# Performance work log

Hardware: AMD Instinct MI355X
Metric: run time of the kernel (lower is better)

Reference implementation:

```python
import jax, jax.numpy as jnp
import numpy as np

BUCKET_SIZE = 64  # init kwarg bucket_size
DIM = 64          # init kwarg dim (per-head dim, used for scaling)


def setup_inputs() -> dict:
    key = jax.random.key(0)
    kq, kk = jax.random.split(key)
    q = jax.random.normal(kq, (32, 8192, 64), dtype=jnp.float32)
    k = jax.random.normal(kk, (32, 8192, 64), dtype=jnp.float32)
    return {"q": q, "k": k}


def _cumavg(t):
    # cumulative average along the sequence axis (axis=1)
    r = jnp.arange(1, t.shape[1] + 1, dtype=t.dtype)
    return jnp.cumsum(t, axis=1) / r[None, :, None]


def reference(q, k):
    bh, n, d = q.shape
    buckets = n // BUCKET_SIZE
    kv_buckets = k.shape[1] // BUCKET_SIZE

    # bucket the cumulative averages: [bh, buckets, bucket_size, d]
    q_r = _cumavg(q).reshape(bh, buckets, BUCKET_SIZE, d)
    k_r = _cumavg(k).reshape(bh, kv_buckets, BUCKET_SIZE, d)

    sq = q_r[:, :, 0]                                   # [bh, buckets, d]
    sk = k_r.sum(axis=2)                                # [bh, kv_buckets, d]
    sk = jnp.pad(sk, ((0, 0), (1, 0), (0, 0)))          # pad one zero bucket row at front

    R = jnp.einsum('bie,bje->bij', sq, sk) * (DIM ** -0.5)  # [bh, buckets, kv_buckets+1]

    rows = jnp.arange(buckets)[:, None]
    cols = jnp.arange(kv_buckets + 1)[None, :]
    neg = -jnp.finfo(R.dtype).max
    # masked_fill: for row i, columns i+1..buckets set to -max (cols > rows)
    R = jnp.where(cols > rows, neg, R)
    R = jax.nn.softmax(R, axis=-1)
    # tril(diagonal=-1): keep entries with col < row
    R = jnp.where(cols < rows, R, jnp.zeros((), R.dtype))
    return R
```

## Files before the change

kernel.cpp:

```cpp
#include <hip/hip_runtime.h>
#include <cstddef>

constexpr int BH = 32;
constexpr int N  = 8192;
constexpr int D  = 64;
constexpr int BK = 64;
constexpr int NB = 128;
constexpr int NC = 129;

typedef float v4f __attribute__((ext_vector_type(4)));

__global__ __launch_bounds__(256) void kA(const float* __restrict__ q,
                                          const float* __restrict__ k,
                                          float* __restrict__ qsum,
                                          float* __restrict__ ksum,
                                          float* __restrict__ kw,
                                          float* __restrict__ qfirst,
                                          float* __restrict__ W) {
  const int j = blockIdx.x, b = blockIdx.y;
  const int tid  = threadIdx.x;
  const int f    = tid & 15;
  const int rr   = tid >> 4;
  const int w    = tid >> 6;
  const int lane = tid & 63;
  const int base = j * BK;
  const size_t ob = ((size_t)b * NB + j) * D;

  const v4f* q4 = (const v4f*)(q + ((size_t)b * N + base) * D);
  const v4f* k4 = (const v4f*)(k + ((size_t)b * N + base) * D);

  v4f vq[4], vk[4];
#pragma unroll
  for (int p = 0; p < 4; ++p) vq[p] = __builtin_nontemporal_load(&q4[(16 * p + rr) * 16 + f]);
#pragma unroll
  for (int p = 0; p < 4; ++p) vk[p] = __builtin_nontemporal_load(&k4[(16 * p + rr) * 16 + f]);

  float x = 1.0f / (float)(base + lane + 1);
#pragma unroll
  for (int s = 1; s < 64; s <<= 1) {
    const float y = __shfl_down(x, s, 64);
    if (lane + s < 64) x += y;
  }
  float tw[4];
#pragma unroll
  for (int p = 0; p < 4; ++p) tw[p] = __shfl(x, 16 * p + rr, 64);

  float aq[4] = {0, 0, 0, 0}, ak[4] = {0, 0, 0, 0}, aw[4] = {0, 0, 0, 0};
#pragma unroll
  for (int p = 0; p < 4; ++p) {
    aq[0] += vq[p].x; aq[1] += vq[p].y; aq[2] += vq[p].z; aq[3] += vq[p].w;
    ak[0] += vk[p].x; ak[1] += vk[p].y; ak[2] += vk[p].z; ak[3] += vk[p].w;
    aw[0] += vk[p].x * tw[p]; aw[1] += vk[p].y * tw[p];
    aw[2] += vk[p].z * tw[p]; aw[3] += vk[p].w * tw[p];
  }

#pragma unroll
  for (int c = 0; c < 4; ++c) {
    aq[c] += __shfl_xor(aq[c], 16, 64); aq[c] += __shfl_xor(aq[c], 32, 64);
    ak[c] += __shfl_xor(ak[c], 16, 64); ak[c] += __shfl_xor(ak[c], 32, 64);
    aw[c] += __shfl_xor(aw[c], 16, 64); aw[c] += __shfl_xor(aw[c], 32, 64);
  }

  __shared__ float red[3][4][D];
  if (lane < 16) {
    ((float4*)&red[0][w][0])[f] = make_float4(aq[0], aq[1], aq[2], aq[3]);
    ((float4*)&red[1][w][0])[f] = make_float4(ak[0], ak[1], ak[2], ak[3]);
    ((float4*)&red[2][w][0])[f] = make_float4(aw[0], aw[1], aw[2], aw[3]);
  }
  if (rr == 0) {
    ((float4*)(qfirst + ob))[f] = make_float4(vq[0].x, vq[0].y, vq[0].z, vq[0].w);
  }
  if (tid == 0 && b == 0) W[j] = x;
  __syncthreads();

  if (tid < 192) {
    const int arr = tid >> 6, d = tid & 63;
    const float s = red[arr][0][d] + red[arr][1][d] + red[arr][2][d] + red[arr][3][d];
    float* dst = (arr == 0) ? qsum : (arr == 1) ? ksum : kw;
    dst[ob + d] = s;
  }
}

__global__ __launch_bounds__(256) void kB(const float* __restrict__ qsum,
                                          const float* __restrict__ ksum,
                                          const float* __restrict__ kw,
                                          const float* __restrict__ qfirst,
                                          const float* __restrict__ W,
                                          float* __restrict__ sq,
                                          float* __restrict__ skp) {
  const int side = blockIdx.x;
  const int b    = blockIdx.y;
  const int tid  = threadIdx.x;
  const int d    = tid & 63;
  const int jg   = tid >> 6;

  __shared__ float buf[NB * D];
  __shared__ float tot[4 * D];
  __shared__ float Wl[NB];

  const float* src = (side == 0 ? qsum : ksum) + (size_t)b * NB * D;
  {
    const float4* g4 = (const float4*)src;
    float4* l4 = (float4*)buf;
    for (int u = tid; u < NB * D / 4; u += 256) l4[u] = g4[u];
    if (side == 1 && tid < NB) Wl[tid] = W[tid];
  }
  __syncthreads();

  float t0 = 0.0f;
  for (int jj = 0; jj < 32; ++jj) t0 += buf[(jg * 32 + jj) * D + d];
  tot[jg * D + d] = t0;
  __syncthreads();

  float pre = 0.0f;
  for (int g = 0; g < jg; ++g) pre += tot[g * D + d];

  if (side == 0) {
    for (int jj = 0; jj < 32; ++jj) {
      const int j = jg * 32 + jj;
      const size_t o = ((size_t)b * NB + j) * D + d;
      sq[o] = (pre + qfirst[o]) / (float)(j * BK + 1);
      pre += buf[j * D + d];
    }
  } else {
    if (tid < D) skp[(size_t)b * NC * D + tid] = 0.0f;
    for (int jj = 0; jj < 32; ++jj) {
      const int j = jg * 32 + jj;
      const size_t o = ((size_t)b * NB + j) * D + d;
      skp[((size_t)b * NC + j + 1) * D + d] = pre * Wl[j] + kw[o];
      pre += buf[j * D + d];
    }
  }
}

__global__ __launch_bounds__(256) void kC(const float* __restrict__ sq,
                                          const float* __restrict__ skp,
                                          float* __restrict__ out) {
  const int tile = blockIdx.x, b = blockIdx.y;
  const int tid = threadIdx.x;
  const int jp = tid & 63, rep = tid >> 6;
  const int T0 = tile * 8;
  const int rows = T0 + 8;

  __shared__ float skpS[NB * D];
  __shared__ float sqs[8 * D];

  {
    const float4* g4 = (const float4*)(skp + (size_t)b * NC * D);
    for (int u = tid; u < rows * 16; u += 256) {
      const int row = u >> 4, f = u & 15;
      ((float4*)skpS)[row * 16 + ((f + row) & 15)] = g4[u];
    }
    if (tid < 128)
      ((float4*)sqs)[tid] = ((const float4*)(sq + ((size_t)b * NB + T0) * D))[tid];
  }
  __syncthreads();

  float acc0[2] = {0, 0}, acc1[2] = {0, 0};
  const float4* sk4 = (const float4*)skpS;
  const float4* sq4 = (const float4*)sqs;
#pragma unroll
  for (int d4 = 0; d4 < 16; ++d4) {
    const int slot = (d4 + jp) & 15;
    const float4 k0 = sk4[jp * 16 + slot];
    const float4 k1 = sk4[(jp + 64) * 16 + slot];
#pragma unroll
    for (int ii = 0; ii < 2; ++ii) {
      const float4 s = sq4[(rep * 2 + ii) * 16 + d4];
      acc0[ii] += s.x * k0.x + s.y * k0.y + s.z * k0.z + s.w * k0.w;
      acc1[ii] += s.x * k1.x + s.y * k1.y + s.z * k1.z + s.w * k1.w;
    }
  }

#pragma unroll
  for (int ii = 0; ii < 2; ++ii) {
    const int i = T0 + rep * 2 + ii;
    const int j0 = jp, j1 = jp + 64;
    const float v0 = acc0[ii] * 0.125f, v1 = acc1[ii] * 0.125f;
    const bool val0 = (j0 <= i), val1 = (j1 <= i);
    float m = fmaxf(val0 ? v0 : -3.402823466e38f, val1 ? v1 : -3.402823466e38f);
#pragma unroll
    for (int s = 1; s < 64; s <<= 1) m = fmaxf(m, __shfl_xor(m, s, 64));
    const float e0 = val0 ? __expf(v0 - m) : 0.0f;
    const float e1 = val1 ? __expf(v1 - m) : 0.0f;
    float ss = e0 + e1;
#pragma unroll
    for (int s = 1; s < 64; s <<= 1) ss += __shfl_xor(ss, s, 64);
    const float rden = 1.0f / ss;
    float* orow = out + ((size_t)b * NB + i) * NC;
    orow[j0] = (j0 < i) ? e0 * rden : 0.0f;
    orow[j1] = (j1 < i) ? e1 * rden : 0.0f;
    if (jp == 0) orow[128] = 0.0f;
  }
}

extern "C" void kernel_launch(void* const* d_in, const int* in_sizes, int n_in,
                              void* d_out, int out_size, void* d_ws, size_t ws_size,
                              hipStream_t stream) {
  const float* q = (const float*)d_in[0];
  const float* k = (const float*)d_in[1];
  float* out = (float*)d_out;

  float* ws     = (float*)d_ws;
  float* qsum   = ws;
  float* ksum   = qsum   + (size_t)BH * NB * D;
  float* kw     = ksum   + (size_t)BH * NB * D;
  float* qfirst = kw     + (size_t)BH * NB * D;
  float* sq     = qfirst + (size_t)BH * NB * D;
  float* skp    = sq     + (size_t)BH * NB * D;
  float* W      = skp    + (size_t)BH * NC * D;

  kA<<<dim3(NB, BH), 256, 0, stream>>>(q, k, qsum, ksum, kw, qfirst, W);
  kB<<<dim3(2, BH), 256, 0, stream>>>(qsum, ksum, kw, qfirst, W, sq, skp);
  kC<<<dim3(16, BH), 256, 0, stream>>>(sq, skp, out);
}
```

Measured before the change: 149.2 us.

## Fuse prefix-scan kernel into softmax kernel, recomputing prefix per tile

Merges the bucket prefix-sum kernel into the score/softmax kernel. Each tile block now scans only the bucket rows it needs and writes sq and the padded sk straight into shared memory, skipping the global round trip and one launch. The cost is redundant prefix work across the 16 tiles per head, since later tiles rescan up to the full 128 rows. The scan also runs as serial per-thread loops with uncoalesced-ish global reads.

```diff
diff --git a/kernel.cpp b/kernel.cpp
--- a/kernel.cpp
+++ b/kernel.cpp
@@ -81,81 +81,69 @@
   }
 }
 
-__global__ __launch_bounds__(256) void kB(const float* __restrict__ qsum,
-                                          const float* __restrict__ ksum,
-                                          const float* __restrict__ kw,
-                                          const float* __restrict__ qfirst,
-                                          const float* __restrict__ W,
-                                          float* __restrict__ sq,
-                                          float* __restrict__ skp) {
-  const int side = blockIdx.x;
-  const int b    = blockIdx.y;
-  const int tid  = threadIdx.x;
-  const int d    = tid & 63;
-  const int jg   = tid >> 6;
-
-  __shared__ float buf[NB * D];
-  __shared__ float tot[4 * D];
-  __shared__ float Wl[NB];
-
-  const float* src = (side == 0 ? qsum : ksum) + (size_t)b * NB * D;
-  {
-    const float4* g4 = (const float4*)src;
-    float4* l4 = (float4*)buf;
-    for (int u = tid; u < NB * D / 4; u += 256) l4[u] = g4[u];
-    if (side == 1 && tid < NB) Wl[tid] = W[tid];
-  }
-  __syncthreads();
-
-  float t0 = 0.0f;
-  for (int jj = 0; jj < 32; ++jj) t0 += buf[(jg * 32 + jj) * D + d];
-  tot[jg * D + d] = t0;
-  __syncthreads();
-
-  float pre = 0.0f;
-  for (int g = 0; g < jg; ++g) pre += tot[g * D + d];
-
-  if (side == 0) {
-    for (int jj = 0; jj < 32; ++jj) {
-      const int j = jg * 32 + jj;
-      const size_t o = ((size_t)b * NB + j) * D + d;
-      sq[o] = (pre + qfirst[o]) / (float)(j * BK + 1);
-      pre += buf[j * D + d];
-    }
-  } else {
-    if (tid < D) skp[(size_t)b * NC * D + tid] = 0.0f;
-    for (int jj = 0; jj < 32; ++jj) {
-      const int j = jg * 32 + jj;
-      const size_t o = ((size_t)b * NB + j) * D + d;
-      skp[((size_t)b * NC + j + 1) * D + d] = pre * Wl[j] + kw[o];
-      pre += buf[j * D + d];
-    }
-  }
-}
-
-__global__ __launch_bounds__(256) void kC(const float* __restrict__ sq,
-                                          const float* __restrict__ skp,
-                                          float* __restrict__ out) {
+__global__ __launch_bounds__(256) void kBC(const float* __restrict__ qsum,
+                                           const float* __restrict__ ksum,
+                                           const float* __restrict__ kw,
+                                           const float* __restrict__ qfirst,
+                                           const float* __restrict__ W,
+                                           float* __restrict__ out) {
   const int tile = blockIdx.x, b = blockIdx.y;
   const int tid = threadIdx.x;
-  const int jp = tid & 63, rep = tid >> 6;
   const int T0 = tile * 8;
-  const int rows = T0 + 8;
+  const int Rneed = T0 + 8;
 
   __shared__ float skpS[NB * D];
   __shared__ float sqs[8 * D];
-
-  {
-    const float4* g4 = (const float4*)(skp + (size_t)b * NC * D);
-    for (int u = tid; u < rows * 16; u += 256) {
-      const int row = u >> 4, f = u & 15;
-      ((float4*)skpS)[row * 16 + ((f + row) & 15)] = g4[u];
+  __shared__ float chq[4 * D];
+  __shared__ float chk[4 * D];
+  __shared__ float Wl[NB];
+
+  const int d = tid & 63;
+  const int g = tid >> 6;
+  const float* qs  = qsum   + (size_t)b * NB * D;
+  const float* ks  = ksum   + (size_t)b * NB * D;
+  const float* kwp = kw     + (size_t)b * NB * D;
+  const float* qf  = qfirst + (size_t)b * NB * D;
+
+  if (tid < NB) Wl[tid] = W[tid];
+  if (tid < D)  skpS[tid] = 0.0f;
+
+  float cq = 0.0f, ck = 0.0f;
+  const int gbase = g * 32;
+  if (gbase < Rneed) {
+    const int rmax = (Rneed - gbase < 32) ? (Rneed - gbase) : 32;
+    for (int jj = 0; jj < rmax; ++jj) {
+      const int r = gbase + jj;
+      cq += qs[r * D + d];
+      ck += ks[r * D + d];
     }
-    if (tid < 128)
-      ((float4*)sqs)[tid] = ((const float4*)(sq + ((size_t)b * NB + T0) * D))[tid];
-  }
+  }
+  chq[g * D + d] = cq;
+  chk[g * D + d] = ck;
   __syncthreads();
 
+  float pq = 0.0f, pk = 0.0f;
+  for (int gg = 0; gg < g; ++gg) { pq += chq[gg * D + d]; pk += chk[gg * D + d]; }
+
+  if (gbase < Rneed) {
+    const int rmax = (Rneed - gbase < 32) ? (Rneed - gbase) : 32;
+    for (int jj = 0; jj < rmax; ++jj) {
+      const int r = gbase + jj;
+      const float qv = qs[r * D + d];
+      const float kv = ks[r * D + d];
+      if ((unsigned)(r - T0) < 8u)
+        sqs[(r - T0) * D + d] = (pq + qf[r * D + d]) / (float)(r * BK + 1);
+      pq += qv;
+      if (r < Rneed - 1) {
+        const int c = r + 1;
+        skpS[c * D + ((((d >> 2) + c) & 15) << 2) + (d & 3)] = pk * Wl[r] + kwp[r * D + d];
+      }
+      pk += kv;
+    }
+  }
+  __syncthreads();
+
+  const int jp = tid & 63, rep = tid >> 6;
   float acc0[2] = {0, 0}, acc1[2] = {0, 0};
   const float4* sk4 = (const float4*)skpS;
   const float4* sq4 = (const float4*)sqs;
@@ -206,11 +194,8 @@
   float* ksum   = qsum   + (size_t)BH * NB * D;
   float* kw     = ksum   + (size_t)BH * NB * D;
   float* qfirst = kw     + (size_t)BH * NB * D;
-  float* sq     = qfirst + (size_t)BH * NB * D;
-  float* skp    = sq     + (size_t)BH * NB * D;
-  float* W      = skp    + (size_t)BH * NC * D;
+  float* W      = qfirst + (size_t)BH * NB * D;
 
   kA<<<dim3(NB, BH), 256, 0, stream>>>(q, k, qsum, ksum, kw, qfirst, W);
-  kB<<<dim3(2, BH), 256, 0, stream>>>(qsum, ksum, kw, qfirst, W, sq, skp);
-  kC<<<dim3(16, BH), 256, 0, stream>>>(sq, skp, out);
+  kBC<<<dim3(16, BH), 256, 0, stream>>>(qsum, ksum, kw, qfirst, W, out);
 }
```

Measured after the change: 164.3 us. +10.2%, slower.
